# Kernel tuning notes

Measured on AMD Instinct MI355X. Metric: run time of the kernel, lower is better.

The kernel has to match this reference:

```python
import jax, jax.numpy as jnp
import numpy as np

NEG = -1000000.0  # mask fill value used by the torch module

def setup_inputs() -> dict:
    key = jax.random.key(0)
    ks = jax.random.split(key, 7)
    B, Tq, Tk, Din, H, Dv = 16, 128, 256, 64, 256, 256
    return {
        "queries": jax.random.normal(ks[0], (B, Tq, Din), dtype=jnp.float32),
        "keys": jax.random.normal(ks[1], (B, Tk, Din), dtype=jnp.float32),
        "values": jax.random.normal(ks[2], (B, Tk, Dv), dtype=jnp.float32),
        "valid_lens": jax.random.randint(ks[3], (B,), 0, Tk, dtype=jnp.int32),
        "wq": jax.random.normal(ks[4], (Din, H), dtype=jnp.float32) * 0.05,
        "wk": jax.random.normal(ks[5], (Din, H), dtype=jnp.float32) * 0.05,
        "wv": jax.random.normal(ks[6], (H,), dtype=jnp.float32) * 0.05,
    }

def reference(queries, keys, values, valid_lens, wq, wk, wv):
    # Project queries and keys to num_hiddens
    q = jnp.einsum("bqd,dh->bqh", queries, wq)       # [B,Tq,H]
    k = jnp.einsum("bkd,dh->bkh", keys, wk)          # [B,Tk,H]
    # Additive features [B,Tq,Tk,H] -> tanh -> scalar score via wv
    feats = jnp.tanh(q[:, :, None, :] + k[:, None, :, :])
    scores = jnp.einsum("bqkh,h->bqk", feats, wv)    # [B,Tq,Tk]
    # Masked softmax over last axis; valid_lens [B] broadcasts over Tq
    Tk = scores.shape[-1]
    mask = jnp.arange(Tk)[None, None, :] < valid_lens[:, None, None]
    scores = jnp.where(mask, scores, NEG)
    attn = jax.nn.softmax(scores, axis=-1)           # [B,Tq,Tk]
    return jnp.einsum("bqk,bkv->bqv", attn, values)  # [B,Tq,Dv]
```

## Files before the change

### kernel.cpp

```cpp
#include <hip/hip_runtime.h>

#define B_  16
#define TQ  128
#define TK  256
#define DIN 64
#define H_  256
#define DV  256
#define HT  8
#define QT  4
#define NW  8
#define NEG -1000000.0f

#define SCALE  2.8853900817779268f
#define LOG2E  1.4426950408889634f

__device__ inline float fast_exp2(float x) { return __builtin_amdgcn_exp2f(x); }
__device__ inline float fast_rcp(float x)  { return __builtin_amdgcn_rcpf(x); }

__global__ __launch_bounds__(256) void proj_k_kernel(
    const float* __restrict__ keys, const float* __restrict__ wk,
    float* __restrict__ EkT, const int* __restrict__ valid_lens)
{
    int b  = blockIdx.x >> 5;
    int h0 = (blockIdx.x & 31) * HT;
    int t  = threadIdx.x;
    int vlC = (valid_lens[b] + 63) & ~63;
    if (t >= vlC) return;
    const float4* krow4 = (const float4*)(keys + (size_t)(b * TK + t) * DIN);
    float acc[HT];
    #pragma unroll
    for (int hh = 0; hh < HT; ++hh) acc[hh] = 0.f;
    #pragma unroll 4
    for (int d4 = 0; d4 < DIN / 4; ++d4) {
        float4 kd = krow4[d4];
        const float* wrow = wk + 4 * d4 * H_ + h0;
        #pragma unroll
        for (int hh = 0; hh < HT; ++hh) acc[hh] = fmaf(kd.x, wrow[hh], acc[hh]);
        #pragma unroll
        for (int hh = 0; hh < HT; ++hh) acc[hh] = fmaf(kd.y, wrow[H_ + hh], acc[hh]);
        #pragma unroll
        for (int hh = 0; hh < HT; ++hh) acc[hh] = fmaf(kd.z, wrow[2 * H_ + hh], acc[hh]);
        #pragma unroll
        for (int hh = 0; hh < HT; ++hh) acc[hh] = fmaf(kd.w, wrow[3 * H_ + hh], acc[hh]);
    }
    #pragma unroll
    for (int hh = 0; hh < HT; ++hh)
        EkT[(b * H_ + h0 + hh) * TK + t] = fast_exp2(acc[hh] * SCALE);
}

__device__ inline float waveMax(float v) {
    #pragma unroll
    for (int off = 32; off > 0; off >>= 1) v = fmaxf(v, __shfl_xor(v, off, 64));
    return v;
}
__device__ inline float waveSum(float v) {
    #pragma unroll
    for (int off = 32; off > 0; off >>= 1) v += __shfl_xor(v, off, 64);
    return v;
}

__global__ __launch_bounds__(512, 4) void attn_kernel(
    const float* __restrict__ queries, const float* __restrict__ wq,
    const float* __restrict__ EkT,
    const float* __restrict__ values, const int* __restrict__ valid_lens,
    const float* __restrict__ wv, float* __restrict__ out)
{
    __shared__ float2 eq2[2][H_];
    __shared__ float  wvL[H_];
    __shared__ float  scoreP[NW][QT][TK];
    __shared__ float  attnT[TK][QT];

    int bx  = blockIdx.x;
    int xcd = bx & 7;
    int i   = bx >> 3;
    int b   = xcd + 8 * (i & 1);
    int q0  = (i >> 1) * QT;
    int t   = threadIdx.x;
    int w   = t >> 6, l = t & 63;
    int vl  = valid_lens[b];

    {
        int h = t & 255, rp = t >> 8;
        const float* qbase = queries + (size_t)(b * TQ + q0 + rp * 2) * DIN;
        float a0 = 0.f, a1 = 0.f;
        #pragma unroll
        for (int d = 0; d < DIN; ++d) {
            float ww = wq[d * H_ + h];
            a0 = fmaf(qbase[d],       ww, a0);
            a1 = fmaf(qbase[DIN + d], ww, a1);
        }
        eq2[rp][h] = make_float2(fast_exp2(a0 * SCALE), fast_exp2(a1 * SCALE));
        if (t < 256) wvL[h] = wv[h];
    }
    __syncthreads();

    {
        const float4* ek4 = (const float4*)(EkT + (size_t)b * H_ * TK);
        float4 s0 = {0,0,0,0}, s1 = {0,0,0,0}, s2 = {0,0,0,0}, s3 = {0,0,0,0};
        int h0 = w * (H_ / NW);

        auto body = [&](int h, float4 kv) {
            float2 eA  = eq2[0][h];
            float2 eB  = eq2[1][h];
            float  wvh = wvL[h];
            float r;
            r = fast_rcp(fmaf(eA.x, kv.x, 1.f)); s0.x = fmaf(wvh, r, s0.x);
            r = fast_rcp(fmaf(eA.x, kv.y, 1.f)); s0.y = fmaf(wvh, r, s0.y);
            r = fast_rcp(fmaf(eA.x, kv.z, 1.f)); s0.z = fmaf(wvh, r, s0.z);
            r = fast_rcp(fmaf(eA.x, kv.w, 1.f)); s0.w = fmaf(wvh, r, s0.w);
            r = fast_rcp(fmaf(eA.y, kv.x, 1.f)); s1.x = fmaf(wvh, r, s1.x);
            r = fast_rcp(fmaf(eA.y, kv.y, 1.f)); s1.y = fmaf(wvh, r, s1.y);
            r = fast_rcp(fmaf(eA.y, kv.z, 1.f)); s1.z = fmaf(wvh, r, s1.z);
            r = fast_rcp(fmaf(eA.y, kv.w, 1.f)); s1.w = fmaf(wvh, r, s1.w);
            r = fast_rcp(fmaf(eB.x, kv.x, 1.f)); s2.x = fmaf(wvh, r, s2.x);
            r = fast_rcp(fmaf(eB.x, kv.y, 1.f)); s2.y = fmaf(wvh, r, s2.y);
            r = fast_rcp(fmaf(eB.x, kv.z, 1.f)); s2.z = fmaf(wvh, r, s2.z);
            r = fast_rcp(fmaf(eB.x, kv.w, 1.f)); s2.w = fmaf(wvh, r, s2.w);
            r = fast_rcp(fmaf(eB.y, kv.x, 1.f)); s3.x = fmaf(wvh, r, s3.x);
            r = fast_rcp(fmaf(eB.y, kv.y, 1.f)); s3.y = fmaf(wvh, r, s3.y);
            r = fast_rcp(fmaf(eB.y, kv.z, 1.f)); s3.z = fmaf(wvh, r, s3.z);
            r = fast_rcp(fmaf(eB.y, kv.w, 1.f)); s3.w = fmaf(wvh, r, s3.w);
        };

        float4 kv = ek4[(size_t)h0 * (TK / 4) + l];
        #pragma unroll 2
        for (int hh = 0; hh < H_ / NW - 1; ++hh) {
            float4 kvn = ek4[(size_t)(h0 + hh + 1) * (TK / 4) + l];
            body(h0 + hh, kv);
            kv = kvn;
        }
        body(h0 + H_ / NW - 1, kv);

        ((float4*)&scoreP[w][0][0])[l] = s0;
        ((float4*)&scoreP[w][1][0])[l] = s1;
        ((float4*)&scoreP[w][2][0])[l] = s2;
        ((float4*)&scoreP[w][3][0])[l] = s3;
    }
    __syncthreads();

    if (t < 64 * QT) {
        int r = w;
        float W = waveSum(wvL[l] + wvL[l + 64] + wvL[l + 128] + wvL[l + 192]);
        float4 v = {0, 0, 0, 0};
        #pragma unroll
        for (int s = 0; s < NW; ++s) {
            float4 ps = ((const float4*)&scoreP[s][r][0])[l];
            v.x += ps.x; v.y += ps.y; v.z += ps.z; v.w += ps.w;
        }
        int k0 = 4 * l;
        v.x = (k0     < vl) ? fmaf(-2.f, v.x, W) : NEG;
        v.y = (k0 + 1 < vl) ? fmaf(-2.f, v.y, W) : NEG;
        v.z = (k0 + 2 < vl) ? fmaf(-2.f, v.z, W) : NEG;
        v.w = (k0 + 3 < vl) ? fmaf(-2.f, v.w, W) : NEG;
        float m  = waveMax(fmaxf(fmaxf(v.x, v.y), fmaxf(v.z, v.w)));
        float p0 = fast_exp2((v.x - m) * LOG2E);
        float p1 = fast_exp2((v.y - m) * LOG2E);
        float p2 = fast_exp2((v.z - m) * LOG2E);
        float p3 = fast_exp2((v.w - m) * LOG2E);
        float dr = fast_rcp(waveSum(p0 + p1 + p2 + p3));
        attnT[k0    ][r] = p0 * dr;
        attnT[k0 + 1][r] = p1 * dr;
        attnT[k0 + 2][r] = p2 * dr;
        attnT[k0 + 3][r] = p3 * dr;
    }
    __syncthreads();

    {
        int half = t >> 8, v = t & 255;
        int kLim = (vl == 0) ? TK : vl;
        int kBeg = half * (TK / 2);
        int kEnd = min(kBeg + TK / 2, kLim);
        const float*  vcol = values + (size_t)b * TK * DV + v;
        const float4* at4  = (const float4*)attnT;
        float o0 = 0.f, o1 = 0.f, o2 = 0.f, o3 = 0.f;
        #pragma unroll 4
        for (int k = kBeg; k < kEnd; ++k) {
            float  vv = vcol[k * DV];
            float4 a  = at4[k];
            o0 = fmaf(a.x, vv, o0);
            o1 = fmaf(a.y, vv, o1);
            o2 = fmaf(a.z, vv, o2);
            o3 = fmaf(a.w, vv, o3);
        }
        if (half == 1) {
            scoreP[0][0][v] = o0;
            scoreP[0][1][v] = o1;
            scoreP[0][2][v] = o2;
            scoreP[0][3][v] = o3;
        }
        __syncthreads();
        if (half == 0) {
            float* orow = out + (size_t)(b * TQ + q0) * DV + v;
            orow[0]      = o0 + scoreP[0][0][v];
            orow[DV]     = o1 + scoreP[0][1][v];
            orow[2 * DV] = o2 + scoreP[0][2][v];
            orow[3 * DV] = o3 + scoreP[0][3][v];
        }
    }
}

extern "C" void kernel_launch(void* const* d_in, const int* in_sizes, int n_in,
                              void* d_out, int out_size, void* d_ws, size_t ws_size,
                              hipStream_t stream) {
    const float* queries    = (const float*)d_in[0];
    const float* keys       = (const float*)d_in[1];
    const float* values     = (const float*)d_in[2];
    const int*   valid_lens = (const int*)  d_in[3];
    const float* wq         = (const float*)d_in[4];
    const float* wk         = (const float*)d_in[5];
    const float* wv         = (const float*)d_in[6];
    float* out = (float*)d_out;

    float* EkT = (float*)d_ws;

    proj_k_kernel<<<B_ * (H_ / HT), 256, 0, stream>>>(keys, wk, EkT, valid_lens);
    attn_kernel<<<B_ * (TQ / QT), 512, 0, stream>>>(queries, wq, EkT, values,
                                                    valid_lens, wv, out);
}
```

Baseline: 101.2 us.

## Move query projection into projection kernel and read eq/wv directly from global

The exp-transformed query projection moves out of the attention kernel and into the key-projection kernel as 512 extra blocks, which write a float4-per-h workspace. The attention kernel then drops its shared-memory staging and the first barrier, loading eq and wv per h straight from global memory using a wave-uniform index via readfirstlane, so these loads can be scalar or broadcast. The aim is to shorten the attention kernel's prologue and cut its LDS use. The cost is an extra workspace round trip, and the main loop now depends on global or scalar loads instead of LDS reads.

```diff
diff --git a/kernel.cpp b/kernel.cpp
--- a/kernel.cpp
+++ b/kernel.cpp
@@ -17,35 +17,57 @@
 __device__ inline float fast_exp2(float x) { return __builtin_amdgcn_exp2f(x); }
 __device__ inline float fast_rcp(float x)  { return __builtin_amdgcn_rcpf(x); }
 
-__global__ __launch_bounds__(256) void proj_k_kernel(
+__global__ __launch_bounds__(256) void proj_kernel(
     const float* __restrict__ keys, const float* __restrict__ wk,
-    float* __restrict__ EkT, const int* __restrict__ valid_lens)
+    const float* __restrict__ queries, const float* __restrict__ wq,
+    float* __restrict__ EkT, float4* __restrict__ EqW,
+    const int* __restrict__ valid_lens)
 {
-    int b  = blockIdx.x >> 5;
-    int h0 = (blockIdx.x & 31) * HT;
+    int bx = blockIdx.x;
     int t  = threadIdx.x;
-    int vlC = (valid_lens[b] + 63) & ~63;
-    if (t >= vlC) return;
-    const float4* krow4 = (const float4*)(keys + (size_t)(b * TK + t) * DIN);
-    float acc[HT];
-    #pragma unroll
-    for (int hh = 0; hh < HT; ++hh) acc[hh] = 0.f;
-    #pragma unroll 4
-    for (int d4 = 0; d4 < DIN / 4; ++d4) {
-        float4 kd = krow4[d4];
-        const float* wrow = wk + 4 * d4 * H_ + h0;
-        #pragma unroll
-        for (int hh = 0; hh < HT; ++hh) acc[hh] = fmaf(kd.x, wrow[hh], acc[hh]);
-        #pragma unroll
-        for (int hh = 0; hh < HT; ++hh) acc[hh] = fmaf(kd.y, wrow[H_ + hh], acc[hh]);
-        #pragma unroll
-        for (int hh = 0; hh < HT; ++hh) acc[hh] = fmaf(kd.z, wrow[2 * H_ + hh], acc[hh]);
-        #pragma unroll
-        for (int hh = 0; hh < HT; ++hh) acc[hh] = fmaf(kd.w, wrow[3 * H_ + hh], acc[hh]);
-    }
-    #pragma unroll
-    for (int hh = 0; hh < HT; ++hh)
-        EkT[(b * H_ + h0 + hh) * TK + t] = fast_exp2(acc[hh] * SCALE);
+    if (bx < 512) {
+        int b  = bx >> 5;
+        int h0 = (bx & 31) * HT;
+        int vlC = (valid_lens[b] + 63) & ~63;
+        if (t >= vlC) return;
+        const float4* krow4 = (const float4*)(keys + (size_t)(b * TK + t) * DIN);
+        float acc[HT];
+        #pragma unroll
+        for (int hh = 0; hh < HT; ++hh) acc[hh] = 0.f;
+        #pragma unroll 4
+        for (int d4 = 0; d4 < DIN / 4; ++d4) {
+            float4 kd = krow4[d4];
+            const float* wrow = wk + 4 * d4 * H_ + h0;
+            #pragma unroll
+            for (int hh = 0; hh < HT; ++hh) acc[hh] = fmaf(kd.x, wrow[hh], acc[hh]);
+            #pragma unroll
+            for (int hh = 0; hh < HT; ++hh) acc[hh] = fmaf(kd.y, wrow[H_ + hh], acc[hh]);
+            #pragma unroll
+            for (int hh = 0; hh < HT; ++hh) acc[hh] = fmaf(kd.z, wrow[2 * H_ + hh], acc[hh]);
+            #pragma unroll
+            for (int hh = 0; hh < HT; ++hh) acc[hh] = fmaf(kd.w, wrow[3 * H_ + hh], acc[hh]);
+        }
+        #pragma unroll
+        for (int hh = 0; hh < HT; ++hh)
+            EkT[(b * H_ + h0 + hh) * TK + t] = fast_exp2(acc[hh] * SCALE);
+    } else {
+        int i = bx - 512;
+        int b = i >> 5;
+        int g = i & 31;
+        const float* qbase = queries + (size_t)(b * TQ + 4 * g) * DIN;
+        float a0 = 0.f, a1 = 0.f, a2 = 0.f, a3 = 0.f;
+        #pragma unroll
+        for (int d = 0; d < DIN; ++d) {
+            float ww = wq[d * H_ + t];
+            a0 = fmaf(qbase[d],           ww, a0);
+            a1 = fmaf(qbase[DIN + d],     ww, a1);
+            a2 = fmaf(qbase[2 * DIN + d], ww, a2);
+            a3 = fmaf(qbase[3 * DIN + d], ww, a3);
+        }
+        EqW[(size_t)(b * 32 + g) * H_ + t] =
+            make_float4(fast_exp2(a0 * SCALE), fast_exp2(a1 * SCALE),
+                        fast_exp2(a2 * SCALE), fast_exp2(a3 * SCALE));
+    }
 }
 
 __device__ inline float waveMax(float v) {
@@ -60,66 +82,49 @@
 }
 
 __global__ __launch_bounds__(512, 4) void attn_kernel(
-    const float* __restrict__ queries, const float* __restrict__ wq,
-    const float* __restrict__ EkT,
+    const float4* __restrict__ EqW, const float* __restrict__ EkT,
     const float* __restrict__ values, const int* __restrict__ valid_lens,
     const float* __restrict__ wv, float* __restrict__ out)
 {
-    __shared__ float2 eq2[2][H_];
-    __shared__ float  wvL[H_];
-    __shared__ float  scoreP[NW][QT][TK];
-    __shared__ float  attnT[TK][QT];
+    __shared__ float scoreP[NW][QT][TK];
+    __shared__ float attnT[TK][QT];
 
     int bx  = blockIdx.x;
     int xcd = bx & 7;
     int i   = bx >> 3;
     int b   = xcd + 8 * (i & 1);
-    int q0  = (i >> 1) * QT;
+    int g   = i >> 1;
+    int q0  = g * QT;
     int t   = threadIdx.x;
     int w   = t >> 6, l = t & 63;
     int vl  = valid_lens[b];
 
     {
-        int h = t & 255, rp = t >> 8;
-        const float* qbase = queries + (size_t)(b * TQ + q0 + rp * 2) * DIN;
-        float a0 = 0.f, a1 = 0.f;
-        #pragma unroll
-        for (int d = 0; d < DIN; ++d) {
-            float ww = wq[d * H_ + h];
-            a0 = fmaf(qbase[d],       ww, a0);
-            a1 = fmaf(qbase[DIN + d], ww, a1);
-        }
-        eq2[rp][h] = make_float2(fast_exp2(a0 * SCALE), fast_exp2(a1 * SCALE));
-        if (t < 256) wvL[h] = wv[h];
-    }
-    __syncthreads();
-
-    {
+        const float4* eqb = EqW + (size_t)(b * 32 + g) * H_;
         const float4* ek4 = (const float4*)(EkT + (size_t)b * H_ * TK);
+        int h0 = __builtin_amdgcn_readfirstlane(w) * (H_ / NW);
         float4 s0 = {0,0,0,0}, s1 = {0,0,0,0}, s2 = {0,0,0,0}, s3 = {0,0,0,0};
-        int h0 = w * (H_ / NW);
 
         auto body = [&](int h, float4 kv) {
-            float2 eA  = eq2[0][h];
-            float2 eB  = eq2[1][h];
-            float  wvh = wvL[h];
+            float4 eq  = eqb[h];
+            float  wvh = wv[h];
             float r;
-            r = fast_rcp(fmaf(eA.x, kv.x, 1.f)); s0.x = fmaf(wvh, r, s0.x);
-            r = fast_rcp(fmaf(eA.x, kv.y, 1.f)); s0.y = fmaf(wvh, r, s0.y);
-            r = fast_rcp(fmaf(eA.x, kv.z, 1.f)); s0.z = fmaf(wvh, r, s0.z);
-            r = fast_rcp(fmaf(eA.x, kv.w, 1.f)); s0.w = fmaf(wvh, r, s0.w);
-            r = fast_rcp(fmaf(eA.y, kv.x, 1.f)); s1.x = fmaf(wvh, r, s1.x);
-            r = fast_rcp(fmaf(eA.y, kv.y, 1.f)); s1.y = fmaf(wvh, r, s1.y);
-            r = fast_rcp(fmaf(eA.y, kv.z, 1.f)); s1.z = fmaf(wvh, r, s1.z);
-            r = fast_rcp(fmaf(eA.y, kv.w, 1.f)); s1.w = fmaf(wvh, r, s1.w);
-            r = fast_rcp(fmaf(eB.x, kv.x, 1.f)); s2.x = fmaf(wvh, r, s2.x);
-            r = fast_rcp(fmaf(eB.x, kv.y, 1.f)); s2.y = fmaf(wvh, r, s2.y);
-            r = fast_rcp(fmaf(eB.x, kv.z, 1.f)); s2.z = fmaf(wvh, r, s2.z);
-            r = fast_rcp(fmaf(eB.x, kv.w, 1.f)); s2.w = fmaf(wvh, r, s2.w);
-            r = fast_rcp(fmaf(eB.y, kv.x, 1.f)); s3.x = fmaf(wvh, r, s3.x);
-            r = fast_rcp(fmaf(eB.y, kv.y, 1.f)); s3.y = fmaf(wvh, r, s3.y);
-            r = fast_rcp(fmaf(eB.y, kv.z, 1.f)); s3.z = fmaf(wvh, r, s3.z);
-            r = fast_rcp(fmaf(eB.y, kv.w, 1.f)); s3.w = fmaf(wvh, r, s3.w);
+            r = fast_rcp(fmaf(eq.x, kv.x, 1.f)); s0.x = fmaf(wvh, r, s0.x);
+            r = fast_rcp(fmaf(eq.x, kv.y, 1.f)); s0.y = fmaf(wvh, r, s0.y);
+            r = fast_rcp(fmaf(eq.x, kv.z, 1.f)); s0.z = fmaf(wvh, r, s0.z);
+            r = fast_rcp(fmaf(eq.x, kv.w, 1.f)); s0.w = fmaf(wvh, r, s0.w);
+            r = fast_rcp(fmaf(eq.y, kv.x, 1.f)); s1.x = fmaf(wvh, r, s1.x);
+            r = fast_rcp(fmaf(eq.y, kv.y, 1.f)); s1.y = fmaf(wvh, r, s1.y);
+            r = fast_rcp(fmaf(eq.y, kv.z, 1.f)); s1.z = fmaf(wvh, r, s1.z);
+            r = fast_rcp(fmaf(eq.y, kv.w, 1.f)); s1.w = fmaf(wvh, r, s1.w);
+            r = fast_rcp(fmaf(eq.z, kv.x, 1.f)); s2.x = fmaf(wvh, r, s2.x);
+            r = fast_rcp(fmaf(eq.z, kv.y, 1.f)); s2.y = fmaf(wvh, r, s2.y);
+            r = fast_rcp(fmaf(eq.z, kv.z, 1.f)); s2.z = fmaf(wvh, r, s2.z);
+            r = fast_rcp(fmaf(eq.z, kv.w, 1.f)); s2.w = fmaf(wvh, r, s2.w);
+            r = fast_rcp(fmaf(eq.w, kv.x, 1.f)); s3.x = fmaf(wvh, r, s3.x);
+            r = fast_rcp(fmaf(eq.w, kv.y, 1.f)); s3.y = fmaf(wvh, r, s3.y);
+            r = fast_rcp(fmaf(eq.w, kv.z, 1.f)); s3.z = fmaf(wvh, r, s3.z);
+            r = fast_rcp(fmaf(eq.w, kv.w, 1.f)); s3.w = fmaf(wvh, r, s3.w);
         };
 
         float4 kv = ek4[(size_t)h0 * (TK / 4) + l];
@@ -140,7 +145,7 @@
 
     if (t < 64 * QT) {
         int r = w;
-        float W = waveSum(wvL[l] + wvL[l + 64] + wvL[l + 128] + wvL[l + 192]);
+        float W = waveSum(wv[l] + wv[l + 64] + wv[l + 128] + wv[l + 192]);
         float4 v = {0, 0, 0, 0};
         #pragma unroll
         for (int s = 0; s < NW; ++s) {
@@ -211,9 +216,10 @@
     const float* wv         = (const float*)d_in[6];
     float* out = (float*)d_out;
 
-    float* EkT = (float*)d_ws;
-
-    proj_k_kernel<<<B_ * (H_ / HT), 256, 0, stream>>>(keys, wk, EkT, valid_lens);
-    attn_kernel<<<B_ * (TQ / QT), 512, 0, stream>>>(queries, wq, EkT, values,
+    float*  EkT = (float*)d_ws;
+    float4* EqW = (float4*)(EkT + (size_t)B_ * H_ * TK);
+
+    proj_kernel<<<1024, 256, 0, stream>>>(keys, wk, queries, wq, EkT, EqW, valid_lens);
+    attn_kernel<<<B_ * (TQ / QT), 512, 0, stream>>>(EqW, EkT, values,
                                                     valid_lens, wv, out);
 }
```

Result: faster. 97.92 us (-3.2%).
